# Optimization experiments

Hardware: AMD Instinct MI355X
Metric: run time of the kernel (lower is better)

## Reference

```python
import jax, jax.numpy as jnp
import numpy as np

N_NODES = 100000
N_EDGES = 1600000
N_GRAPHS = 64
IN_CH = 128
HID = 128
N_CLASSES = 8


def setup_inputs() -> dict:
    key = jax.random.key(0)
    ks = jax.random.split(key, 8)
    x = jax.random.normal(ks[0], (N_NODES, IN_CH), dtype=jnp.float32)
    edge_index = jax.random.randint(ks[1], (2, N_EDGES), 0, N_NODES, dtype=jnp.int64)
    batch = jnp.sort(jax.random.randint(ks[2], (N_NODES,), 0, N_GRAPHS, dtype=jnp.int64))
    s1 = 1.0 / np.sqrt(IN_CH)
    s2 = 1.0 / np.sqrt(HID)
    W1 = jax.random.normal(ks[3], (IN_CH, HID), dtype=jnp.float32) * s1
    b1 = jnp.zeros((HID,), dtype=jnp.float32)
    W2 = jax.random.normal(ks[4], (HID, HID), dtype=jnp.float32) * s2
    b2 = jnp.zeros((HID,), dtype=jnp.float32)
    lin_W = jax.random.normal(ks[5], (HID, N_CLASSES), dtype=jnp.float32) * s2
    lin_b = jnp.zeros((N_CLASSES,), dtype=jnp.float32)
    return {"x": x, "edge_index": edge_index, "batch": batch,
            "W1": W1, "b1": b1, "W2": W2, "b2": b2,
            "lin_W": lin_W, "lin_b": lin_b}


def _gcn_norm(edge_index, n_nodes):
    # add self-loops, compute symmetric normalization coefficients
    loops = jnp.arange(n_nodes, dtype=edge_index.dtype)
    src = jnp.concatenate([edge_index[0], loops])
    dst = jnp.concatenate([edge_index[1], loops])
    ones = jnp.ones(src.shape[0], dtype=jnp.float32)
    deg = jax.ops.segment_sum(ones, dst, num_segments=n_nodes)
    dinv = jnp.where(deg > 0, jax.lax.rsqrt(jnp.maximum(deg, 1.0)), 0.0)
    norm = dinv[src] * dinv[dst]  # [E + N]
    return src, dst, norm


def _gcn_conv(x, W, b, src, dst, norm, n_nodes):
    xw = x @ W                               # [N, H]
    msg = xw[src] * norm[:, None]            # gather + scale, [E+N, H]
    out = jax.ops.segment_sum(msg, dst, num_segments=n_nodes)
    return out + b


def reference(x, edge_index, batch, W1, b1, W2, b2, lin_W, lin_b):
    n = x.shape[0]
    src, dst, norm = _gcn_norm(edge_index, n)
    h = jax.nn.relu(_gcn_conv(x, W1, b1, src, dst, norm, n))
    h = _gcn_conv(h, W2, b2, src, dst, norm, n)
    # global mean pool over graphs
    sums = jax.ops.segment_sum(h, batch, num_segments=N_GRAPHS)
    cnts = jax.ops.segment_sum(jnp.ones(n, dtype=h.dtype), batch, num_segments=N_GRAPHS)
    pooled = sums / jnp.maximum(cnts, 1.0)[:, None]
    return pooled @ lin_W + lin_b
```

## Files before the change

kernel.cpp:

```cpp
#include <hip/hip_runtime.h>
#include <hip/hip_fp16.h>
#include <cstdint>
#include <cstddef>

#define NNODES 100000
#define NEDGES 1600000
#define NGRAPHS 64
#define BSHIFT 7
#define BRANGE 128
#define NB 782
#define CAP 4096
#define NZ NB
#define LP 136
#define NAB 25000

typedef short short8v __attribute__((ext_vector_type(8)));
typedef float float4v __attribute__((ext_vector_type(4)));

__device__ inline short f2h_s(float f) {
    __half h = __float2half(f);
    return __builtin_bit_cast(short, h);
}
__device__ inline ushort f2h_u(float f) {
    __half h = __float2half(f);
    return __builtin_bit_cast(ushort, h);
}
__device__ inline __half2 u2h2(uint u) { return __builtin_bit_cast(__half2, u); }
__device__ inline uint h22u(__half2 h) { return __builtin_bit_cast(uint, h); }


__global__ __launch_bounds__(256) void k_setup(int* __restrict__ zb,
                                               const float* __restrict__ W1,
                                               const float* __restrict__ W2,
                                               short8v* __restrict__ o1,
                                               short8v* __restrict__ o2,
                                               const int* __restrict__ batch,
                                               int* __restrict__ gstart,
                                               int* __restrict__ gend) {
    int b = blockIdx.x, t = threadIdx.x;
    if (b < 4) {
        int i = b * 256 + t;
        if (i < NZ) zb[i] = 0;
    } else if (b < 6) {
        const float* W = (b == 5) ? W2 : W1;
        short8v* o = (b == 5) ? o2 : o1;
        for (int s = t; s < 2048; s += 256) {
            int p = s >> 6, l = s & 63;
            int kb = (p >> 3) * 32 + ((l >> 4) * 8);
            int j = (p & 7) * 16 + (l & 15);
            short8v v;
            #pragma unroll
            for (int i = 0; i < 8; ++i)
                v[i] = f2h_s(W[(size_t)(kb + i) * 128 + j]);
            o[s] = v;
        }
    } else {
        int i = (b - 6) * 256 + t;
        if (i < NNODES) {
            int bb = batch[i];
            if (i == 0 || batch[i - 1] != bb) gstart[bb] = i;
            if (i == NNODES - 1 || batch[i + 1] != bb) gend[bb] = i + 1;
        }
    }
}


#define P1_EPT 16
__global__ __launch_bounds__(512) void k_bscatter(const int* __restrict__ src,
                                                  const int* __restrict__ dst,
                                                  int* __restrict__ bcur,
                                                  uint* __restrict__ pairs, int E) {
    __shared__ int h[NB];
    __shared__ int base[NB];
    int t = threadIdx.x;
    long long c0 = (long long)blockIdx.x * 8192;
    if (c0 >= E) return;
    for (int i = t; i < NB; i += 512) h[i] = 0;
    __syncthreads();
    int myb[P1_EPT], mylp[P1_EPT];
    uint myv[P1_EPT];
    #pragma unroll
    for (int k = 0; k < P1_EPT; ++k) {
        long long e = c0 + t + k * 512;
        if (e < E) {
            int d = dst[e];
            myv[k] = (uint)src[e] | ((uint)(d & (BRANGE - 1)) << 24);
            myb[k] = d >> BSHIFT;
            mylp[k] = atomicAdd(&h[myb[k]], 1);
        } else myb[k] = -1;
    }
    __syncthreads();
    for (int i = t; i < NB; i += 512)
        base[i] = h[i] ? atomicAdd(&bcur[i], h[i]) : 0;
    __syncthreads();
    #pragma unroll
    for (int k = 0; k < P1_EPT; ++k)
        if (myb[k] >= 0) {
            int pos = base[myb[k]] + mylp[k];
            if (pos < CAP)
                pairs[(size_t)myb[k] * CAP + pos] = myv[k];
        }
}


__global__ __launch_bounds__(512) void k_build(const uint* __restrict__ pairs,
                                               const int* __restrict__ bcur,
                                               int2* __restrict__ nr,
                                               float* __restrict__ dinv,
                                               int* __restrict__ csr, int N) {
    __shared__ int h[256];
    __shared__ int sh[256];
    __shared__ int cur[BRANGE];
    int b = blockIdx.x, t = threadIdx.x;
    if (t < 256) h[t] = 0;
    __syncthreads();
    const int p0 = b * CAP;
    const int cntb = min(bcur[b], CAP);
    for (int p = t; p < cntb; p += 512)
        atomicAdd(&h[pairs[p0 + p] >> 24], 1);
    __syncthreads();
    int myh = (t < 256) ? h[t] : 0;
    if (t < 256) sh[t] = myh;
    __syncthreads();
    #pragma unroll
    for (int d = 1; d < 256; d <<= 1) {
        int val = (t >= d && t < 256) ? sh[t - d] : 0;
        __syncthreads();
        if (t < 256) sh[t] += val;
        __syncthreads();
    }
    int node = (b << BSHIFT) + t;
    if (t < BRANGE) {
        int excl = sh[t] - myh;
        cur[t] = p0 + excl;
        if (node < N) {
            nr[node] = make_int2(p0 + excl, p0 + excl + myh);
            dinv[node] = rsqrtf((float)(myh + 1));
        }
    }
    __syncthreads();
    for (int p = t; p < cntb; p += 512) {
        uint pr = pairs[p0 + p];
        int pos = atomicAdd(&cur[pr >> 24], 1);
        csr[pos] = (int)(pr & 0x00FFFFFFu);
    }
}


__global__ __launch_bounds__(256) void k_gemm_f32(const float4* __restrict__ X4,
                                                  const short8v* __restrict__ wf,
                                                  const float* __restrict__ dinv,
                                                  ushort* __restrict__ Y, int n) {
    __shared__ ushort ht[16 * LP];
    const int t = threadIdx.x;
    const int lane = t & 63;
    const int w = t >> 6;
    const int row0 = blockIdx.x * 16;

    #pragma unroll
    for (int s = t; s < 16 * 32; s += 256) {
        int row = s >> 5, q = s & 31;
        float4 v = X4[(size_t)(row0 + row) * 32 + q];
        ushort2 h0 = make_ushort2(f2h_u(v.x), f2h_u(v.y));
        ushort2 h1 = make_ushort2(f2h_u(v.z), f2h_u(v.w));
        *(ushort2*)&ht[row * LP + q * 4] = h0;
        *(ushort2*)&ht[row * LP + q * 4 + 2] = h1;
    }
    __syncthreads();

    float4v acc[2];
    acc[0] = (float4v)0.f;
    acc[1] = (float4v)0.f;
    const int arow = lane & 15;
    const int ct0 = w * 2;
    #pragma unroll
    for (int kk = 0; kk < 4; ++kk) {
        short8v a = *(const short8v*)&ht[arow * LP + kk * 32 + ((lane >> 4) * 8)];
        acc[0] = __builtin_amdgcn_mfma_f32_16x16x32_f16(a, wf[(kk * 8 + ct0) * 64 + lane],
                                                        acc[0], 0, 0, 0);
        acc[1] = __builtin_amdgcn_mfma_f32_16x16x32_f16(a, wf[(kk * 8 + ct0 + 1) * 64 + lane],
                                                        acc[1], 0, 0, 0);
    }
    const int orow = row0 + ((lane >> 4) << 2);
    #pragma unroll
    for (int r = 0; r < 4; ++r) {
        int row = orow + r;
        float dr = dinv[row];
        Y[(size_t)row * 128 + ct0 * 16 + (lane & 15)]       = f2h_u(acc[0][r] * dr);
        Y[(size_t)row * 128 + (ct0 + 1) * 16 + (lane & 15)] = f2h_u(acc[1][r] * dr);
    }
}


__global__ __launch_bounds__(512) void k_agg_gemm(const uint* __restrict__ msg,
                                                  const float* __restrict__ dinv,
                                                  const int2* __restrict__ nr,
                                                  const int* __restrict__ csr,
                                                  const float* __restrict__ bias,
                                                  const short8v* __restrict__ wf,
                                                  ushort* __restrict__ Y, int n) {
    __shared__ ushort ht[16 * LP];
    const int t = threadIdx.x;
    const int lane = t & 63;
    const int w = t >> 6;
    const int row0 = blockIdx.x * 16;
    const float bx = bias[lane * 2];
    const float by = bias[lane * 2 + 1];

    #pragma unroll
    for (int i = 0; i < 2; ++i) {
        const int r = w * 2 + i;
        const int wid = row0 + r;
        __half2 a0 = u2h2(msg[(size_t)wid * 64 + lane]);
        __half2 a1 = u2h2(0u), a2 = u2h2(0u);
        const int2 rg = nr[wid];
        const int e0 = rg.x, e1 = rg.y;
        for (int e = e0; e < e1; e += 64) {
            int me = e + lane;
            int sidx = (me < e1) ? csr[me] : 0;
            int cnt = min(64, e1 - e);
            for (int kb = 0; kb < cnt; kb += 6) {
                int lim = cnt - 1;
                int s0 = __shfl(sidx, min(kb + 0, lim));
                int s1 = __shfl(sidx, min(kb + 1, lim));
                int s2 = __shfl(sidx, min(kb + 2, lim));
                int s3 = __shfl(sidx, min(kb + 3, lim));
                int s4 = __shfl(sidx, min(kb + 4, lim));
                int s5 = __shfl(sidx, min(kb + 5, lim));
                uint u0 = msg[(size_t)s0 * 64 + lane];
                uint u1 = msg[(size_t)s1 * 64 + lane];
                uint u2 = msg[(size_t)s2 * 64 + lane];
                uint u3 = msg[(size_t)s3 * 64 + lane];
                uint u4 = msg[(size_t)s4 * 64 + lane];
                uint u5 = msg[(size_t)s5 * 64 + lane];
                u1 = (kb + 1 < cnt) ? u1 : 0u;
                u2 = (kb + 2 < cnt) ? u2 : 0u;
                u3 = (kb + 3 < cnt) ? u3 : 0u;
                u4 = (kb + 4 < cnt) ? u4 : 0u;
                u5 = (kb + 5 < cnt) ? u5 : 0u;
                a0 = __hadd2(a0, u2h2(u0));
                a1 = __hadd2(a1, u2h2(u1));
                a2 = __hadd2(a2, u2h2(u2));
                a0 = __hadd2(a0, u2h2(u3));
                a1 = __hadd2(a1, u2h2(u4));
                a2 = __hadd2(a2, u2h2(u5));
            }
        }
        __half2 acc = __hadd2(__hadd2(a0, a1), a2);
        float2 f = __half22float2(acc);
        float dd = dinv[wid];
        float ax = fmaxf(f.x * dd + bx, 0.f);
        float ay = fmaxf(f.y * dd + by, 0.f);
        *(uint*)&ht[r * LP + lane * 2] = h22u(__floats2half2_rn(ax, ay));
    }
    __syncthreads();

    float4v acc = (float4v)0.f;
    const int arow = lane & 15;
    #pragma unroll
    for (int kk = 0; kk < 4; ++kk) {
        short8v a = *(const short8v*)&ht[arow * LP + kk * 32 + ((lane >> 4) * 8)];
        acc = __builtin_amdgcn_mfma_f32_16x16x32_f16(a, wf[(kk * 8 + w) * 64 + lane],
                                                     acc, 0, 0, 0);
    }
    const int orow = row0 + ((lane >> 4) << 2);
    #pragma unroll
    for (int r = 0; r < 4; ++r) {
        int row = orow + r;
        float dr = dinv[row];
        Y[(size_t)row * 128 + w * 16 + (lane & 15)] = f2h_u(acc[r] * dr);
    }
}


__global__ __launch_bounds__(256) void k_agg_pool(const uint* __restrict__ msg,
                                                  const float* __restrict__ dinv,
                                                  const int2* __restrict__ nr,
                                                  const int* __restrict__ csr,
                                                  const int* __restrict__ batch,
                                                  float* __restrict__ pA,
                                                  float* __restrict__ pB) {
    __shared__ float red[4][128];
    __shared__ int selw[4];
    const int blk = blockIdx.x;
    const int t = threadIdx.x;
    const int lane = t & 63;
    const int w = t >> 6;
    const int wid = blk * 4 + w;

    __half2 a0 = u2h2(msg[(size_t)wid * 64 + lane]);
    __half2 a1 = u2h2(0u), a2 = u2h2(0u);
    const int2 rg = nr[wid];
    const int e0 = rg.x, e1 = rg.y;
    for (int e = e0; e < e1; e += 64) {
        int me = e + lane;
        int sidx = (me < e1) ? csr[me] : 0;
        int cnt = min(64, e1 - e);
        for (int kb = 0; kb < cnt; kb += 6) {
            int lim = cnt - 1;
            int s0 = __shfl(sidx, min(kb + 0, lim));
            int s1 = __shfl(sidx, min(kb + 1, lim));
            int s2 = __shfl(sidx, min(kb + 2, lim));
            int s3 = __shfl(sidx, min(kb + 3, lim));
            int s4 = __shfl(sidx, min(kb + 4, lim));
            int s5 = __shfl(sidx, min(kb + 5, lim));
            uint u0 = msg[(size_t)s0 * 64 + lane];
            uint u1 = msg[(size_t)s1 * 64 + lane];
            uint u2 = msg[(size_t)s2 * 64 + lane];
            uint u3 = msg[(size_t)s3 * 64 + lane];
            uint u4 = msg[(size_t)s4 * 64 + lane];
            uint u5 = msg[(size_t)s5 * 64 + lane];
            u1 = (kb + 1 < cnt) ? u1 : 0u;
            u2 = (kb + 2 < cnt) ? u2 : 0u;
            u3 = (kb + 3 < cnt) ? u3 : 0u;
            u4 = (kb + 4 < cnt) ? u4 : 0u;
            u5 = (kb + 5 < cnt) ? u5 : 0u;
            a0 = __hadd2(a0, u2h2(u0));
            a1 = __hadd2(a1, u2h2(u1));
            a2 = __hadd2(a2, u2h2(u2));
            a0 = __hadd2(a0, u2h2(u3));
            a1 = __hadd2(a1, u2h2(u4));
            a2 = __hadd2(a2, u2h2(u5));
        }
    }
    __half2 acc = __hadd2(__hadd2(a0, a1), a2);
    float2 f = __half22float2(acc);
    float dd = dinv[wid];
    red[w][lane * 2] = f.x * dd;
    red[w][lane * 2 + 1] = f.y * dd;
    if (lane == 0) selw[w] = (batch[wid] != batch[blk * 4]) ? 1 : 0;
    __syncthreads();
    if (t < 128) {
        float a = 0.f, b = 0.f;
        #pragma unroll
        for (int ww = 0; ww < 4; ++ww) {
            float v = red[ww][t];
            if (selw[ww]) b += v; else a += v;
        }
        pA[(size_t)blk * 128 + t] = a;
        if (selw[0] | selw[1] | selw[2] | selw[3])
            pB[(size_t)blk * 128 + t] = b;
    }
}


__global__ __launch_bounds__(512) void k_final(const float* __restrict__ pA,
                                               const float* __restrict__ pB,
                                               const int* __restrict__ batch,
                                               const int* __restrict__ gstart,
                                               const int* __restrict__ gend,
                                               const float* __restrict__ b2,
                                               const float* __restrict__ linW,
                                               const float* __restrict__ linb,
                                               float* __restrict__ out) {
    __shared__ float sq[4][128];
    __shared__ float red[128][8];
    int g = blockIdx.x;
    int t = threadIdx.x;
    int c = t & 127;
    int q = t >> 7;
    int b0 = gstart[g] >> 2;
    int b1 = (gend[g] - 1) >> 2;
    float v = 0.f;
    #pragma unroll 4
    for (int b = b0 + 1 + q; b <= b1; b += 4)
        v += pA[(size_t)b * 128 + c];
    if (q == 0)
        v += ((batch[b0 * 4] != g) ? pB : pA)[(size_t)b0 * 128 + c];
    sq[q][c] = v;
    __syncthreads();
    if (t < 128) {
        float sv = sq[0][t] + sq[1][t] + sq[2][t] + sq[3][t];
        float cnt = (float)(gend[g] - gstart[g]);
        sv = sv / fmaxf(cnt, 1.0f) + b2[t];
        #pragma unroll
        for (int k = 0; k < 8; ++k) red[t][k] = sv * linW[(size_t)t * 8 + k];
    }
    __syncthreads();
    #pragma unroll
    for (int st = 64; st > 0; st >>= 1) {
        if (t < st) {
            #pragma unroll
            for (int k = 0; k < 8; ++k) red[t][k] += red[t + st][k];
        }
        __syncthreads();
    }
    if (t < 8) out[(size_t)g * 8 + t] = red[0][t] + linb[t];
}


extern "C" void kernel_launch(void* const* d_in, const int* in_sizes, int n_in,
                              void* d_out, int out_size, void* d_ws, size_t ws_size,
                              hipStream_t stream) {
    const float* x     = (const float*)d_in[0];
    const int*   ei    = (const int*)d_in[1];
    const int*   batch = (const int*)d_in[2];
    const float* W1    = (const float*)d_in[3];
    const float* b1    = (const float*)d_in[4];
    const float* W2    = (const float*)d_in[5];
    const float* b2    = (const float*)d_in[6];
    const float* linW  = (const float*)d_in[7];
    const float* linb  = (const float*)d_in[8];
    float* out = (float*)d_out;

    const int N = NNODES, E = NEDGES;
    const int* src = ei;
    const int* dst = ei + E;

    char* ws = (char*)d_ws;
    uint*  bufA16 = (uint*)ws;     ws += (size_t)N * 64 * 4;
    uint*  bufH16 = (uint*)ws;     ws += (size_t)N * 64 * 4;
    float* dinv   = (float*)ws;    ws += (size_t)N * 4;
    int2*  nr     = (int2*)ws;     ws += (size_t)N * 8;
    int*   csr    = (int*)ws;      ws += (size_t)NB * CAP * 4;
    int*   bcur   = (int*)ws;      ws += NB * 4;
    int*   gstart = (int*)ws;      ws += NGRAPHS * 4;
    int*   gend   = (int*)ws;      ws += NGRAPHS * 4;
    short8v* wf1  = (short8v*)ws;  ws += 2048 * 16;
    short8v* wf2  = (short8v*)ws;  ws += 2048 * 16;
    float* pA     = (float*)ws;    ws += (size_t)NAB * 128 * 4;
    float* pB     = (float*)ws;    ws += (size_t)NAB * 128 * 4;
    uint*  pairs  = (uint*)bufH16;

    const int B = 256;

    k_setup<<<397, B, 0, stream>>>(bcur, W1, W2, wf1, wf2, batch, gstart, gend);

    k_bscatter<<<(E + 8191) / 8192, 512, 0, stream>>>(src, dst, bcur, pairs, E);
    k_build<<<NB, 512, 0, stream>>>(pairs, bcur, nr, dinv, csr, N);

    k_gemm_f32<<<N / 16, B, 0, stream>>>((const float4*)x, wf1, dinv, (ushort*)bufA16, N);

    k_agg_gemm<<<N / 16, 512, 0, stream>>>(bufA16, dinv, nr, csr, b1, wf2,
                                           (ushort*)bufH16, N);

    k_agg_pool<<<NAB, B, 0, stream>>>(bufH16, dinv, nr, csr, batch, pA, pB);

    k_final<<<NGRAPHS, 512, 0, stream>>>(pA, pB, batch, gstart, gend, b2, linW, linb, out);
}
```

Measured before the change: 194.7 us.

## Store node messages in FP8 and pad CSR rows to multiples of eight

Node feature messages are now written as packed FP8 pairs (two bytes per lane) instead of FP16 pairs, halving the gather traffic in both aggregation kernels. Accumulation moves to FP32 after a hardware FP8-to-float conversion. CSR neighbor lists are padded to multiples of eight, with the padding pointing at an extra all-zero sentinel row, so the gather loop runs 8-wide with no bounds masking. The pairs buffer gets its own workspace region instead of aliasing the second message buffer. The cost is much lower precision of intermediate activations, plus extra padded gathers and extra workspace.

```diff
diff --git a/kernel.cpp b/kernel.cpp
--- a/kernel.cpp
+++ b/kernel.cpp
@@ -16,6 +16,7 @@
 
 typedef short short8v __attribute__((ext_vector_type(8)));
 typedef float float4v __attribute__((ext_vector_type(4)));
+typedef float float2v __attribute__((ext_vector_type(2)));
 
 __device__ inline short f2h_s(float f) {
     __half h = __float2half(f);
@@ -25,8 +26,14 @@
     __half h = __float2half(f);
     return __builtin_bit_cast(ushort, h);
 }
-__device__ inline __half2 u2h2(uint u) { return __builtin_bit_cast(__half2, u); }
 __device__ inline uint h22u(__half2 h) { return __builtin_bit_cast(uint, h); }
+
+__device__ inline float2v fp8x2_f32(uint u) {
+    return __builtin_amdgcn_cvt_pk_f32_fp8((int)u, false);
+}
+__device__ inline ushort f32_fp8x2(float a, float b) {
+    return (ushort)__builtin_amdgcn_cvt_pk_fp8_f32(a, b, 0, false);
+}
 
 
 __global__ __launch_bounds__(256) void k_setup(int* __restrict__ zb,
@@ -34,6 +41,8 @@
                                                const float* __restrict__ W2,
                                                short8v* __restrict__ o1,
                                                short8v* __restrict__ o2,
+                                               uint* __restrict__ rowNA,
+                                               uint* __restrict__ rowNH,
                                                const int* __restrict__ batch,
                                                int* __restrict__ gstart,
                                                int* __restrict__ gend) {
@@ -54,8 +63,11 @@
                 v[i] = f2h_s(W[(size_t)(kb + i) * 128 + j]);
             o[s] = v;
         }
+    } else if (b == 6) {
+        if (t < 32) rowNA[t] = 0u;
+        else if (t < 64) rowNH[t - 32] = 0u;
     } else {
-        int i = (b - 6) * 256 + t;
+        int i = (b - 7) * 256 + t;
         if (i < NNODES) {
             int bb = batch[i];
             if (i == 0 || batch[i - 1] != bb) gstart[bb] = i;
@@ -111,6 +123,7 @@
     __shared__ int h[256];
     __shared__ int sh[256];
     __shared__ int cur[BRANGE];
+    __shared__ int pend[BRANGE];
     int b = blockIdx.x, t = threadIdx.x;
     if (t < 256) h[t] = 0;
     __syncthreads();
@@ -120,7 +133,8 @@
         atomicAdd(&h[pairs[p0 + p] >> 24], 1);
     __syncthreads();
     int myh = (t < 256) ? h[t] : 0;
-    if (t < 256) sh[t] = myh;
+    int p8 = (myh + 7) & ~7;
+    if (t < 256) sh[t] = p8;
     __syncthreads();
     #pragma unroll
     for (int d = 1; d < 256; d <<= 1) {
@@ -131,10 +145,11 @@
     }
     int node = (b << BSHIFT) + t;
     if (t < BRANGE) {
-        int excl = sh[t] - myh;
-        cur[t] = p0 + excl;
+        int st = p0 + sh[t] - p8;
+        cur[t] = st;
+        pend[t] = st + p8;
         if (node < N) {
-            nr[node] = make_int2(p0 + excl, p0 + excl + myh);
+            nr[node] = make_int2(st, st + p8);
             dinv[node] = rsqrtf((float)(myh + 1));
         }
     }
@@ -144,13 +159,18 @@
         int pos = atomicAdd(&cur[pr >> 24], 1);
         csr[pos] = (int)(pr & 0x00FFFFFFu);
     }
+    __syncthreads();
+    if (t < BRANGE) {
+        for (int pos = cur[t]; pos < pend[t]; ++pos)
+            csr[pos] = N;
+    }
 }
 
 
 __global__ __launch_bounds__(256) void k_gemm_f32(const float4* __restrict__ X4,
                                                   const short8v* __restrict__ wf,
                                                   const float* __restrict__ dinv,
-                                                  ushort* __restrict__ Y, int n) {
+                                                  ushort* __restrict__ Y8, int n) {
     __shared__ ushort ht[16 * LP];
     const int t = threadIdx.x;
     const int lane = t & 63;
@@ -186,19 +206,75 @@
     for (int r = 0; r < 4; ++r) {
         int row = orow + r;
         float dr = dinv[row];
-        Y[(size_t)row * 128 + ct0 * 16 + (lane & 15)]       = f2h_u(acc[0][r] * dr);
-        Y[(size_t)row * 128 + (ct0 + 1) * 16 + (lane & 15)] = f2h_u(acc[1][r] * dr);
-    }
-}
-
-
-__global__ __launch_bounds__(512) void k_agg_gemm(const uint* __restrict__ msg,
+        #pragma unroll
+        for (int j = 0; j < 2; ++j) {
+            float a = acc[j][r] * dr;
+            float b = __shfl_xor(a, 1);
+            if (!(lane & 1))
+                Y8[(size_t)row * 64 + (ct0 + j) * 8 + ((lane & 15) >> 1)] = f32_fp8x2(a, b);
+        }
+    }
+}
+
+
+__device__ inline void agg_node(const ushort* __restrict__ msg,
+                                const int* __restrict__ csr,
+                                int e0, int e1, int lane, uint uself,
+                                float& outx, float& outy) {
+    float2v fs = fp8x2_f32(uself);
+    float ax0 = fs[0], ay0 = fs[1];
+    float ax1 = 0.f, ay1 = 0.f, ax2 = 0.f, ay2 = 0.f, ax3 = 0.f, ay3 = 0.f;
+    for (int e = e0; e < e1; e += 64) {
+        int me = e + lane;
+        int sidx = (me < e1) ? csr[me] : NNODES;
+        int cnt = min(64, e1 - e);
+        for (int kb = 0; kb < cnt; kb += 8) {
+            int s0 = __shfl(sidx, kb + 0);
+            int s1 = __shfl(sidx, kb + 1);
+            int s2 = __shfl(sidx, kb + 2);
+            int s3 = __shfl(sidx, kb + 3);
+            int s4 = __shfl(sidx, kb + 4);
+            int s5 = __shfl(sidx, kb + 5);
+            int s6 = __shfl(sidx, kb + 6);
+            int s7 = __shfl(sidx, kb + 7);
+            uint u0 = msg[(size_t)s0 * 64 + lane];
+            uint u1 = msg[(size_t)s1 * 64 + lane];
+            uint u2 = msg[(size_t)s2 * 64 + lane];
+            uint u3 = msg[(size_t)s3 * 64 + lane];
+            uint u4 = msg[(size_t)s4 * 64 + lane];
+            uint u5 = msg[(size_t)s5 * 64 + lane];
+            uint u6 = msg[(size_t)s6 * 64 + lane];
+            uint u7 = msg[(size_t)s7 * 64 + lane];
+            float2v f0 = fp8x2_f32(u0);
+            float2v f1 = fp8x2_f32(u1);
+            float2v f2 = fp8x2_f32(u2);
+            float2v f3 = fp8x2_f32(u3);
+            float2v f4 = fp8x2_f32(u4);
+            float2v f5 = fp8x2_f32(u5);
+            float2v f6 = fp8x2_f32(u6);
+            float2v f7 = fp8x2_f32(u7);
+            ax0 += f0[0]; ay0 += f0[1];
+            ax1 += f1[0]; ay1 += f1[1];
+            ax2 += f2[0]; ay2 += f2[1];
+            ax3 += f3[0]; ay3 += f3[1];
+            ax0 += f4[0]; ay0 += f4[1];
+            ax1 += f5[0]; ay1 += f5[1];
+            ax2 += f6[0]; ay2 += f6[1];
+            ax3 += f7[0]; ay3 += f7[1];
+        }
+    }
+    outx = (ax0 + ax1) + (ax2 + ax3);
+    outy = (ay0 + ay1) + (ay2 + ay3);
+}
+
+
+__global__ __launch_bounds__(512) void k_agg_gemm(const ushort* __restrict__ msg,
                                                   const float* __restrict__ dinv,
                                                   const int2* __restrict__ nr,
                                                   const int* __restrict__ csr,
                                                   const float* __restrict__ bias,
                                                   const short8v* __restrict__ wf,
-                                                  ushort* __restrict__ Y, int n) {
+                                                  ushort* __restrict__ Y8, int n) {
     __shared__ ushort ht[16 * LP];
     const int t = threadIdx.x;
     const int lane = t & 63;
@@ -211,46 +287,13 @@
     for (int i = 0; i < 2; ++i) {
         const int r = w * 2 + i;
         const int wid = row0 + r;
-        __half2 a0 = u2h2(msg[(size_t)wid * 64 + lane]);
-        __half2 a1 = u2h2(0u), a2 = u2h2(0u);
         const int2 rg = nr[wid];
-        const int e0 = rg.x, e1 = rg.y;
-        for (int e = e0; e < e1; e += 64) {
-            int me = e + lane;
-            int sidx = (me < e1) ? csr[me] : 0;
-            int cnt = min(64, e1 - e);
-            for (int kb = 0; kb < cnt; kb += 6) {
-                int lim = cnt - 1;
-                int s0 = __shfl(sidx, min(kb + 0, lim));
-                int s1 = __shfl(sidx, min(kb + 1, lim));
-                int s2 = __shfl(sidx, min(kb + 2, lim));
-                int s3 = __shfl(sidx, min(kb + 3, lim));
-                int s4 = __shfl(sidx, min(kb + 4, lim));
-                int s5 = __shfl(sidx, min(kb + 5, lim));
-                uint u0 = msg[(size_t)s0 * 64 + lane];
-                uint u1 = msg[(size_t)s1 * 64 + lane];
-                uint u2 = msg[(size_t)s2 * 64 + lane];
-                uint u3 = msg[(size_t)s3 * 64 + lane];
-                uint u4 = msg[(size_t)s4 * 64 + lane];
-                uint u5 = msg[(size_t)s5 * 64 + lane];
-                u1 = (kb + 1 < cnt) ? u1 : 0u;
-                u2 = (kb + 2 < cnt) ? u2 : 0u;
-                u3 = (kb + 3 < cnt) ? u3 : 0u;
-                u4 = (kb + 4 < cnt) ? u4 : 0u;
-                u5 = (kb + 5 < cnt) ? u5 : 0u;
-                a0 = __hadd2(a0, u2h2(u0));
-                a1 = __hadd2(a1, u2h2(u1));
-                a2 = __hadd2(a2, u2h2(u2));
-                a0 = __hadd2(a0, u2h2(u3));
-                a1 = __hadd2(a1, u2h2(u4));
-                a2 = __hadd2(a2, u2h2(u5));
-            }
-        }
-        __half2 acc = __hadd2(__hadd2(a0, a1), a2);
-        float2 f = __half22float2(acc);
+        uint uself = msg[(size_t)wid * 64 + lane];
+        float sx, sy;
+        agg_node(msg, csr, rg.x, rg.y, lane, uself, sx, sy);
         float dd = dinv[wid];
-        float ax = fmaxf(f.x * dd + bx, 0.f);
-        float ay = fmaxf(f.y * dd + by, 0.f);
+        float ax = fmaxf(sx * dd + bx, 0.f);
+        float ay = fmaxf(sy * dd + by, 0.f);
         *(uint*)&ht[r * LP + lane * 2] = h22u(__floats2half2_rn(ax, ay));
     }
     __syncthreads();
@@ -268,12 +311,15 @@
     for (int r = 0; r < 4; ++r) {
         int row = orow + r;
         float dr = dinv[row];
-        Y[(size_t)row * 128 + w * 16 + (lane & 15)] = f2h_u(acc[r] * dr);
-    }
-}
-
-
-__global__ __launch_bounds__(256) void k_agg_pool(const uint* __restrict__ msg,
+        float a = acc[r] * dr;
+        float b = __shfl_xor(a, 1);
+        if (!(lane & 1))
+            Y8[(size_t)row * 64 + w * 8 + ((lane & 15) >> 1)] = f32_fp8x2(a, b);
+    }
+}
+
+
+__global__ __launch_bounds__(256) void k_agg_pool(const ushort* __restrict__ msg,
                                                   const float* __restrict__ dinv,
                                                   const int2* __restrict__ nr,
                                                   const int* __restrict__ csr,
@@ -288,46 +334,13 @@
     const int w = t >> 6;
     const int wid = blk * 4 + w;
 
-    __half2 a0 = u2h2(msg[(size_t)wid * 64 + lane]);
-    __half2 a1 = u2h2(0u), a2 = u2h2(0u);
     const int2 rg = nr[wid];
-    const int e0 = rg.x, e1 = rg.y;
-    for (int e = e0; e < e1; e += 64) {
-        int me = e + lane;
-        int sidx = (me < e1) ? csr[me] : 0;
-        int cnt = min(64, e1 - e);
-        for (int kb = 0; kb < cnt; kb += 6) {
-            int lim = cnt - 1;
-            int s0 = __shfl(sidx, min(kb + 0, lim));
-            int s1 = __shfl(sidx, min(kb + 1, lim));
-            int s2 = __shfl(sidx, min(kb + 2, lim));
-            int s3 = __shfl(sidx, min(kb + 3, lim));
-            int s4 = __shfl(sidx, min(kb + 4, lim));
-            int s5 = __shfl(sidx, min(kb + 5, lim));
-            uint u0 = msg[(size_t)s0 * 64 + lane];
-            uint u1 = msg[(size_t)s1 * 64 + lane];
-            uint u2 = msg[(size_t)s2 * 64 + lane];
-            uint u3 = msg[(size_t)s3 * 64 + lane];
-            uint u4 = msg[(size_t)s4 * 64 + lane];
-            uint u5 = msg[(size_t)s5 * 64 + lane];
-            u1 = (kb + 1 < cnt) ? u1 : 0u;
-            u2 = (kb + 2 < cnt) ? u2 : 0u;
-            u3 = (kb + 3 < cnt) ? u3 : 0u;
-            u4 = (kb + 4 < cnt) ? u4 : 0u;
-            u5 = (kb + 5 < cnt) ? u5 : 0u;
-            a0 = __hadd2(a0, u2h2(u0));
-            a1 = __hadd2(a1, u2h2(u1));
-            a2 = __hadd2(a2, u2h2(u2));
-            a0 = __hadd2(a0, u2h2(u3));
-            a1 = __hadd2(a1, u2h2(u4));
-            a2 = __hadd2(a2, u2h2(u5));
-        }
-    }
-    __half2 acc = __hadd2(__hadd2(a0, a1), a2);
-    float2 f = __half22float2(acc);
+    uint uself = msg[(size_t)wid * 64 + lane];
+    float sx, sy;
+    agg_node(msg, csr, rg.x, rg.y, lane, uself, sx, sy);
     float dd = dinv[wid];
-    red[w][lane * 2] = f.x * dd;
-    red[w][lane * 2 + 1] = f.y * dd;
+    red[w][lane * 2] = sx * dd;
+    red[w][lane * 2 + 1] = sy * dd;
     if (lane == 0) selw[w] = (batch[wid] != batch[blk * 4]) ? 1 : 0;
     __syncthreads();
     if (t < 128) {
@@ -408,11 +421,12 @@
     const int* dst = ei + E;
 
     char* ws = (char*)d_ws;
-    uint*  bufA16 = (uint*)ws;     ws += (size_t)N * 64 * 4;
-    uint*  bufH16 = (uint*)ws;     ws += (size_t)N * 64 * 4;
+    ushort* msgA8 = (ushort*)ws;   ws += (size_t)(N + 1) * 128;
+    ushort* msgH8 = (ushort*)ws;   ws += (size_t)(N + 1) * 128;
     float* dinv   = (float*)ws;    ws += (size_t)N * 4;
     int2*  nr     = (int2*)ws;     ws += (size_t)N * 8;
     int*   csr    = (int*)ws;      ws += (size_t)NB * CAP * 4;
+    uint*  pairs  = (uint*)ws;     ws += (size_t)NB * CAP * 4;
     int*   bcur   = (int*)ws;      ws += NB * 4;
     int*   gstart = (int*)ws;      ws += NGRAPHS * 4;
     int*   gend   = (int*)ws;      ws += NGRAPHS * 4;
@@ -420,21 +434,22 @@
     short8v* wf2  = (short8v*)ws;  ws += 2048 * 16;
     float* pA     = (float*)ws;    ws += (size_t)NAB * 128 * 4;
     float* pB     = (float*)ws;    ws += (size_t)NAB * 128 * 4;
-    uint*  pairs  = (uint*)bufH16;
 
     const int B = 256;
 
-    k_setup<<<397, B, 0, stream>>>(bcur, W1, W2, wf1, wf2, batch, gstart, gend);
+    k_setup<<<398, B, 0, stream>>>(bcur, W1, W2, wf1, wf2,
+                                   (uint*)(msgA8 + (size_t)N * 64),
+                                   (uint*)(msgH8 + (size_t)N * 64),
+                                   batch, gstart, gend);
 
     k_bscatter<<<(E + 8191) / 8192, 512, 0, stream>>>(src, dst, bcur, pairs, E);
     k_build<<<NB, 512, 0, stream>>>(pairs, bcur, nr, dinv, csr, N);
 
-    k_gemm_f32<<<N / 16, B, 0, stream>>>((const float4*)x, wf1, dinv, (ushort*)bufA16, N);
-
-    k_agg_gemm<<<N / 16, 512, 0, stream>>>(bufA16, dinv, nr, csr, b1, wf2,
-                                           (ushort*)bufH16, N);
-
-    k_agg_pool<<<NAB, B, 0, stream>>>(bufH16, dinv, nr, csr, batch, pA, pB);
+    k_gemm_f32<<<N / 16, B, 0, stream>>>((const float4*)x, wf1, dinv, msgA8, N);
+
+    k_agg_gemm<<<N / 16, 512, 0, stream>>>(msgA8, dinv, nr, csr, b1, wf2, msgH8, N);
+
+    k_agg_pool<<<NAB, B, 0, stream>>>(msgH8, dinv, nr, csr, batch, pA, pB);
 
     k_final<<<NGRAPHS, 512, 0, stream>>>(pA, pB, batch, gstart, gend, b2, linW, linb, out);
 }
```

Result: faster. 167.8 us (-13.8%).
